# Kernel optimization log

Hardware: AMD Instinct MI355X
Metric: run time of the kernel (lower is better)

The kernel has to match this reference:

```python
import jax, jax.numpy as jnp
import numpy as np

N_EMBD = 1024
N_HEAD = 16
HEAD = N_EMBD // N_HEAD  # 64
N_HIDDEN = 2816          # ((int(2*4*1024/3)-1)//256)*256 + 256
BLOCK_SIZE = 4096
EPS = 1e-5


def rope_cos_sin(T, hd, base=10000.0):
    theta = 1.0 / (base ** (jnp.arange(0, hd, 2, dtype=jnp.float32) / hd))  # (hd/2,)
    idx = jnp.arange(T, dtype=jnp.float32)
    ang = jnp.outer(idx, theta)  # (T, hd/2)
    return jnp.cos(ang), jnp.sin(ang)


def apply_rope(x, cos, sin):
    # x: (B, H, T, hd); rotate interleaved pairs (x0,x1),(x2,x3),...
    xp = x.reshape(*x.shape[:-1], HEAD // 2, 2)
    xe, xo = xp[..., 0], xp[..., 1]
    c = cos[None, None, :, :]
    s = sin[None, None, :, :]
    oe = xe * c - xo * s
    oo = xe * s + xo * c
    return jnp.stack([oe, oo], axis=-1).reshape(x.shape)


def rmsnorm(x, scale):
    ms = jnp.mean(x * x, axis=-1, keepdims=True)
    return scale * (x * jax.lax.rsqrt(ms + EPS))


def setup_inputs() -> dict:
    key = jax.random.key(0)
    ks = jax.random.split(key, 9)
    B, T = 2, 2048
    x = jax.random.normal(ks[0], (B, T, N_EMBD), dtype=jnp.float32)
    y_mask = jax.random.randint(ks[1], (B, 64), 0, 2, dtype=jnp.int32)
    sd = 1.0 / np.sqrt(N_EMBD)
    Wqkv = jax.random.normal(ks[2], (N_EMBD, 3 * N_EMBD), dtype=jnp.float32) * sd
    Wattn_proj = jax.random.normal(ks[3], (N_EMBD, N_EMBD), dtype=jnp.float32) * sd
    scale1 = jnp.ones((N_EMBD,), dtype=jnp.float32)
    scale2 = jnp.ones((N_EMBD,), dtype=jnp.float32)
    Wfc1 = jax.random.normal(ks[4], (N_EMBD, N_HIDDEN), dtype=jnp.float32) * sd
    Wfc2 = jax.random.normal(ks[5], (N_EMBD, N_HIDDEN), dtype=jnp.float32) * sd
    Wmlp_proj = jax.random.normal(ks[6], (N_HIDDEN, N_EMBD), dtype=jnp.float32) / np.sqrt(N_HIDDEN)
    return {"x": x, "y_mask": y_mask, "Wqkv": Wqkv, "Wattn_proj": Wattn_proj,
            "scale1": scale1, "scale2": scale2, "Wfc1": Wfc1, "Wfc2": Wfc2,
            "Wmlp_proj": Wmlp_proj}


def reference(x, y_mask, Wqkv, Wattn_proj, scale1, scale2, Wfc1, Wfc2, Wmlp_proj):
    B, T, C = x.shape
    # ---- attention branch (pre-RMSNorm) ----
    h = rmsnorm(x, scale1)
    qkv = h @ Wqkv  # (B, T, 3C)
    q, k, v = jnp.split(qkv, 3, axis=-1)
    q = q.reshape(B, T, N_HEAD, HEAD).transpose(0, 2, 1, 3)
    k = k.reshape(B, T, N_HEAD, HEAD).transpose(0, 2, 1, 3)
    v = v.reshape(B, T, N_HEAD, HEAD).transpose(0, 2, 1, 3)
    cos, sin = rope_cos_sin(T, HEAD)
    q = apply_rope(q, cos, sin)
    k = apply_rope(k, cos, sin)
    # mixed causal + text-text bidirectional mask
    causal = jnp.tril(jnp.ones((T, T), dtype=bool))  # (T, T)
    ym = y_mask.astype(bool)  # (B, L)
    L = ym.shape[1]
    text = ym[:, :, None] & ym[:, None, :]  # (B, L, L)
    text = jnp.pad(text, ((0, 0), (0, T - L), (0, T - L)))
    mask = jnp.logical_or(causal[None, :, :], text)  # (B, T, T)
    scale = 1.0 / np.sqrt(HEAD)
    scores = jnp.einsum('bhqd,bhkd->bhqk', q, k) * scale
    scores = jnp.where(mask[:, None, :, :], scores, -jnp.inf)
    attn = jax.nn.softmax(scores, axis=-1)
    y = jnp.einsum('bhqk,bhkd->bhqd', attn, v)
    y = y.transpose(0, 2, 1, 3).reshape(B, T, C)
    x = x + y @ Wattn_proj
    # ---- SwiGLU MLP branch (pre-RMSNorm) ----
    h2 = rmsnorm(x, scale2)
    m = jax.nn.silu(h2 @ Wfc1) * (h2 @ Wfc2)
    x = x + m @ Wmlp_proj
    return x
```

## Files before the change

kernel.cpp:

```cpp
#include <hip/hip_runtime.h>
#include <stdint.h>

typedef unsigned short u16;
typedef __attribute__((ext_vector_type(8))) short bf16x8;
typedef __attribute__((ext_vector_type(4))) float f32x4;

__device__ __forceinline__ float b2f(u16 u) {
    union { float f; uint32_t u; } v; v.u = ((uint32_t)u) << 16; return v.f;
}
__device__ __forceinline__ u16 f2b(float f) {
    union { float f; uint32_t u; } v; v.f = f;
    uint32_t r = v.u + 0x7FFFu + ((v.u >> 16) & 1u);
    return (u16)(r >> 16);
}

template <int CTRL>
__device__ __forceinline__ float dppf(float x) {
    union { float f; int i; } u; u.f = x;
    u.i = __builtin_amdgcn_update_dpp(0, u.i, CTRL, 0xF, 0xF, false);
    return u.f;
}
__device__ __forceinline__ float rowmax16(float v) {
    v = fmaxf(v, dppf<0x121>(v));
    v = fmaxf(v, dppf<0x122>(v));
    v = fmaxf(v, dppf<0x124>(v));
    v = fmaxf(v, dppf<0x128>(v));
    return v;
}
__device__ __forceinline__ float rowsum16(float v) {
    v += dppf<0x121>(v);
    v += dppf<0x122>(v);
    v += dppf<0x124>(v);
    v += dppf<0x128>(v);
    return v;
}

__device__ __forceinline__ void stage16(const void* g, void* l) {
    __builtin_amdgcn_global_load_lds(
        (const __attribute__((address_space(1))) uint32_t*)(uintptr_t)g,
        (__attribute__((address_space(3))) uint32_t*)(uint32_t)(uintptr_t)l,
        16, 0, 0);
}

__global__ __launch_bounds__(256) void transpose_all(const float* __restrict__ Wqkv,
                                                     const float* __restrict__ Wattn,
                                                     const float* __restrict__ Wfc1,
                                                     const float* __restrict__ Wfc2,
                                                     const float* __restrict__ Wmlp,
                                                     u16* WtQ, u16* WtA, u16* WtF1,
                                                     u16* WtF2, u16* WtM) {
    __shared__ u16 tile[32][33];
    int id = blockIdx.x;
    const float* src; u16* dst; int R, C;
    if (id < 3072)      {             src = Wqkv;  dst = WtQ;  R = 1024; C = 3072; }
    else if (id < 4096) { id -= 3072; src = Wattn; dst = WtA;  R = 1024; C = 1024; }
    else if (id < 6912) { id -= 4096; src = Wfc1;  dst = WtF1; R = 1024; C = 2816; }
    else if (id < 9728) { id -= 6912; src = Wfc2;  dst = WtF2; R = 1024; C = 2816; }
    else                { id -= 9728; src = Wmlp;  dst = WtM;  R = 2816; C = 1024; }
    const int nbx = C >> 5;
    const int bx = id % nbx, by = id / nbx;
    const int cx = bx * 32, ry = by * 32;
    const int tx = threadIdx.x, ty = threadIdx.y;
    #pragma unroll
    for (int i = 0; i < 32; i += 8)
        tile[ty + i][tx] = f2b(src[(size_t)(ry + ty + i) * C + cx + tx]);
    __syncthreads();
    #pragma unroll
    for (int i = 0; i < 32; i += 8)
        dst[(size_t)(cx + ty + i) * R + ry + tx] = tile[tx][ty + i];
}

__global__ __launch_bounds__(256) void rmsnorm_f32(const float* __restrict__ xin,
                                                   const float* __restrict__ scale,
                                                   u16* __restrict__ out) {
    const int row = blockIdx.x, tid = threadIdx.x;
    const float4 v = ((const float4*)(xin + (size_t)row * 1024))[tid];
    float ss = v.x * v.x + v.y * v.y + v.z * v.z + v.w * v.w;
    #pragma unroll
    for (int d = 32; d; d >>= 1) ss += __shfl_xor(ss, d);
    __shared__ float wsum[4];
    if ((tid & 63) == 0) wsum[tid >> 6] = ss;
    __syncthreads();
    const float r = rsqrtf((wsum[0] + wsum[1] + wsum[2] + wsum[3]) * (1.f / 1024.f) + 1e-5f);
    const float4 sc = ((const float4*)scale)[tid];
    uint2 o;
    o.x = (uint32_t)f2b(v.x * sc.x * r) | ((uint32_t)f2b(v.y * sc.y * r) << 16);
    o.y = (uint32_t)f2b(v.z * sc.z * r) | ((uint32_t)f2b(v.w * sc.w * r) << 16);
    ((uint2*)(out + (size_t)row * 1024))[tid] = o;
}

__global__ __launch_bounds__(256) void rope_kernel(u16* __restrict__ qkv) {
    const int gid = blockIdx.x * 256 + threadIdx.x;
    const int i = gid & 31;
    const int h = (gid >> 5) & 15;
    const int row = gid >> 9;
    const int t = row & 2047;
    const float theta = expf(-(float)i * (9.210340371976184f / 32.0f));
    const float ang = (float)t * theta;
    const float c = cosf(ang), s = sinf(ang);
    const size_t base = (size_t)row * 3072 + h * 64 + 2 * i;
    {
        float xe = b2f(qkv[base]), xo = b2f(qkv[base + 1]);
        qkv[base]     = f2b(xe * c - xo * s);
        qkv[base + 1] = f2b(xe * s + xo * c);
    }
    {
        float xe = b2f(qkv[base + 1024]), xo = b2f(qkv[base + 1025]);
        qkv[base + 1024] = f2b(xe * c - xo * s);
        qkv[base + 1025] = f2b(xe * s + xo * c);
    }
}

template <int EPI>
__global__ __launch_bounds__(256) void gemm_bt(const u16* __restrict__ A,
                                               const u16* __restrict__ Bt,
                                               void* __restrict__ Cout,
                                               const void* __restrict__ Res,
                                               int N, int K) {
    __shared__ __attribute__((aligned(16))) u16 As[2][128 * 32];
    __shared__ __attribute__((aligned(16))) u16 Bs[2][128 * 32];
    const int tid = threadIdx.x;
    const int w = tid >> 6, lane = tid & 63;
    const int quad = lane >> 4, t = lane & 15;
    const int m0 = blockIdx.y * 128, n0 = blockIdx.x * 128;
    const int wm = (w >> 1) * 64, wn = (w & 1) * 64;

    const int srow = w * 16 + (lane >> 2);
    const int scol = (lane & 3) * 8;
    const u16* pA0 = A + (size_t)(m0 + srow) * K + scol;
    const u16* pA1 = pA0 + (size_t)64 * K;
    const u16* pB0 = Bt + (size_t)(n0 + srow) * K + scol;
    const u16* pB1 = pB0 + (size_t)64 * K;

    f32x4 acc[4][4];
    #pragma unroll
    for (int i = 0; i < 4; ++i)
        #pragma unroll
        for (int j = 0; j < 4; ++j) acc[i][j] = (f32x4){0.f, 0.f, 0.f, 0.f};

    for (int kb = 0; kb < K; kb += 64) {
        __syncthreads();
        stage16(pA0 + kb,      (char*)As[0] + w * 1024);
        stage16(pA1 + kb,      (char*)As[0] + 4096 + w * 1024);
        stage16(pB0 + kb,      (char*)Bs[0] + w * 1024);
        stage16(pB1 + kb,      (char*)Bs[0] + 4096 + w * 1024);
        stage16(pA0 + kb + 32, (char*)As[1] + w * 1024);
        stage16(pA1 + kb + 32, (char*)As[1] + 4096 + w * 1024);
        stage16(pB0 + kb + 32, (char*)Bs[1] + w * 1024);
        stage16(pB1 + kb + 32, (char*)Bs[1] + 4096 + w * 1024);
        __syncthreads();
        #pragma unroll
        for (int hf = 0; hf < 2; ++hf) {
            bf16x8 af[4], bfr[4];
            #pragma unroll
            for (int mi = 0; mi < 4; ++mi)
                af[mi] = *(const bf16x8*)((char*)As[hf] + (wm + mi * 16 + t) * 64 + quad * 16);
            #pragma unroll
            for (int ni = 0; ni < 4; ++ni)
                bfr[ni] = *(const bf16x8*)((char*)Bs[hf] + (wn + ni * 16 + t) * 64 + quad * 16);
            #pragma unroll
            for (int mi = 0; mi < 4; ++mi)
                #pragma unroll
                for (int ni = 0; ni < 4; ++ni)
                    acc[mi][ni] = __builtin_amdgcn_mfma_f32_16x16x32_bf16(af[mi], bfr[ni],
                                                                         acc[mi][ni], 0, 0, 0);
        }
    }
    #pragma unroll
    for (int mi = 0; mi < 4; ++mi) {
        const int row0 = m0 + wm + mi * 16 + quad * 4;
        #pragma unroll
        for (int ni = 0; ni < 4; ++ni) {
            const int col = n0 + wn + ni * 16 + t;
            #pragma unroll
            for (int r = 0; r < 4; ++r) {
                const size_t idx = (size_t)(row0 + r) * N + col;
                const float v = acc[mi][ni][r];
                if (EPI == 0) {
                    ((u16*)Cout)[idx] = f2b(v);
                } else if (EPI == 1) {
                    ((float*)Cout)[idx] = v + ((const float*)Res)[idx];
                } else {
                    const float av = b2f(((const u16*)Res)[idx]);
                    ((u16*)Cout)[idx] = f2b((av / (1.f + __expf(-av))) * v);
                }
            }
        }
    }
}

template <int EPI>
__global__ __launch_bounds__(256) void gemm_bt64(const u16* __restrict__ A,
                                                 const u16* __restrict__ Bt,
                                                 void* __restrict__ Cout,
                                                 const float* __restrict__ Res,
                                                 int N, int K) {
    __shared__ __attribute__((aligned(16))) u16 As[2][128 * 32];
    __shared__ __attribute__((aligned(16))) u16 Bs[2][64 * 32];
    const int tid = threadIdx.x;
    const int w = tid >> 6, lane = tid & 63;
    const int quad = lane >> 4, t = lane & 15;
    const int m0 = blockIdx.y * 128, n0 = blockIdx.x * 64;
    const int wm = (w >> 1) * 64, wn = (w & 1) * 32;

    const int srow = w * 16 + (lane >> 2);
    const int scol = (lane & 3) * 8;
    const u16* pA0 = A + (size_t)(m0 + srow) * K + scol;
    const u16* pA1 = pA0 + (size_t)64 * K;
    const u16* pB0 = Bt + (size_t)(n0 + srow) * K + scol;

    f32x4 acc[4][2];
    #pragma unroll
    for (int i = 0; i < 4; ++i)
        #pragma unroll
        for (int j = 0; j < 2; ++j) acc[i][j] = (f32x4){0.f, 0.f, 0.f, 0.f};

    for (int kb = 0; kb < K; kb += 64) {
        __syncthreads();
        stage16(pA0 + kb,      (char*)As[0] + w * 1024);
        stage16(pA1 + kb,      (char*)As[0] + 4096 + w * 1024);
        stage16(pB0 + kb,      (char*)Bs[0] + w * 1024);
        stage16(pA0 + kb + 32, (char*)As[1] + w * 1024);
        stage16(pA1 + kb + 32, (char*)As[1] + 4096 + w * 1024);
        stage16(pB0 + kb + 32, (char*)Bs[1] + w * 1024);
        __syncthreads();
        #pragma unroll
        for (int hf = 0; hf < 2; ++hf) {
            bf16x8 af[4], bfr[2];
            #pragma unroll
            for (int mi = 0; mi < 4; ++mi)
                af[mi] = *(const bf16x8*)((char*)As[hf] + (wm + mi * 16 + t) * 64 + quad * 16);
            #pragma unroll
            for (int ni = 0; ni < 2; ++ni)
                bfr[ni] = *(const bf16x8*)((char*)Bs[hf] + (wn + ni * 16 + t) * 64 + quad * 16);
            #pragma unroll
            for (int mi = 0; mi < 4; ++mi)
                #pragma unroll
                for (int ni = 0; ni < 2; ++ni)
                    acc[mi][ni] = __builtin_amdgcn_mfma_f32_16x16x32_bf16(af[mi], bfr[ni],
                                                                         acc[mi][ni], 0, 0, 0);
        }
    }
    #pragma unroll
    for (int mi = 0; mi < 4; ++mi) {
        const int row0 = m0 + wm + mi * 16 + quad * 4;
        #pragma unroll
        for (int ni = 0; ni < 2; ++ni) {
            const int col = n0 + wn + ni * 16 + t;
            #pragma unroll
            for (int r = 0; r < 4; ++r) {
                const size_t idx = (size_t)(row0 + r) * N + col;
                const float v = acc[mi][ni][r];
                if (EPI == 0) ((u16*)Cout)[idx]   = f2b(v);
                else          ((float*)Cout)[idx] = v + Res[idx];
            }
        }
    }
}

__global__ __launch_bounds__(256) void attn_kernel(const u16* __restrict__ qkv,
                                                   const int* __restrict__ ymask,
                                                   u16* __restrict__ y) {
    const int qt = 31 - blockIdx.x;
    const int h = blockIdx.y, b = blockIdx.z;
    const int tid = threadIdx.x;
    const int w = tid >> 6, lane = tid & 63;
    const int quad = lane >> 4, t = lane & 15;
    const int q0 = qt * 64;

    __shared__ __attribute__((aligned(16))) u16 Ks[64 * 72];
    __shared__ __attribute__((aligned(16))) u16 Vts[64 * 72];
    __shared__ __attribute__((aligned(16))) u16 Ps[4][16 * 72];
    __shared__ int ymL[64];
    if (qt == 0 && tid < 64) ymL[tid] = ymask[b * 64 + tid];

    bf16x8 aQ[2];
    {
        const u16* qp = qkv + (size_t)(b * 2048 + q0 + w * 16 + t) * 3072 + h * 64 + quad * 8;
        aQ[0] = *(const bf16x8*)qp;
        aQ[1] = *(const bf16x8*)(qp + 32);
        #pragma unroll
        for (int i = 0; i < 8; ++i) {
            aQ[0][i] = (short)f2b(b2f((u16)aQ[0][i]) * 0.125f);
            aQ[1][i] = (short)f2b(b2f((u16)aQ[1][i]) * 0.125f);
        }
    }

    const int skey = tid >> 3, sdg = tid & 7;
    const u16* pK = qkv + (size_t)(b * 2048 + skey) * 3072 + h * 64 + sdg * 8 + 1024;
    const int sblk0 = (skey >> 3) ^ sdg;
    const int sblk1 = (4 + (skey >> 3)) ^ sdg;

    f32x4 accO[4] = {(f32x4){0,0,0,0},(f32x4){0,0,0,0},(f32x4){0,0,0,0},(f32x4){0,0,0,0}};
    float mOld[4] = {-INFINITY, -INFINITY, -INFINITY, -INFINITY};
    float lSum[4] = {0.f, 0.f, 0.f, 0.f};

    for (int kb = 0; kb <= qt; ++kb) {
        const u16* pk = pK + (size_t)kb * 196608;
        const uint4 kv0 = *(const uint4*)pk;
        const uint4 vv0 = *(const uint4*)(pk + 1024);
        const uint4 kv1 = *(const uint4*)(pk + 98304);
        const uint4 vv1 = *(const uint4*)(pk + 99328);
        __syncthreads();
        *(uint4*)((char*)Ks + skey * 144 + sdg * 16) = kv0;
        *(uint4*)((char*)Ks + (skey + 32) * 144 + sdg * 16) = kv1;
        {
            const u16* vp0 = (const u16*)&vv0;
            const u16* vp1 = (const u16*)&vv1;
            #pragma unroll
            for (int jj = 0; jj < 8; ++jj) {
                const int row = sdg * 8 + jj;
                Vts[row * 72 + sblk0 * 8 + (skey & 7)] = vp0[jj];
                Vts[row * 72 + sblk1 * 8 + (skey & 7)] = vp1[jj];
            }
        }
        __syncthreads();

        float s[4][4];
        __builtin_amdgcn_s_setprio(1);
        #pragma unroll
        for (int ni = 0; ni < 4; ++ni) {
            bf16x8 bK0 = *(const bf16x8*)((char*)Ks + (ni * 16 + t) * 144 + quad * 16);
            bf16x8 bK1 = *(const bf16x8*)((char*)Ks + (ni * 16 + t) * 144 + 64 + quad * 16);
            f32x4 sa = (f32x4){0.f, 0.f, 0.f, 0.f};
            sa = __builtin_amdgcn_mfma_f32_16x16x32_bf16(aQ[0], bK0, sa, 0, 0, 0);
            sa = __builtin_amdgcn_mfma_f32_16x16x32_bf16(aQ[1], bK1, sa, 0, 0, 0);
            #pragma unroll
            for (int r = 0; r < 4; ++r) s[ni][r] = sa[r];
        }
        __builtin_amdgcn_s_setprio(0);

        if (kb == qt) {
            const int irow = q0 + w * 16 + quad * 4;
            #pragma unroll
            for (int ni = 0; ni < 4; ++ni)
                #pragma unroll
                for (int r = 0; r < 4; ++r) {
                    const int i = irow + r, j = kb * 64 + ni * 16 + t;
                    const bool ok = (j <= i) || (qt == 0 && ymL[i & 63] && ymL[j & 63]);
                    if (!ok) s[ni][r] = -INFINITY;
                }
        }

        float alpha[4];
        bool upd = false;
        #pragma unroll
        for (int r = 0; r < 4; ++r) {
            float mt = fmaxf(fmaxf(s[0][r], s[1][r]), fmaxf(s[2][r], s[3][r]));
            mt = rowmax16(mt);
            const float mNew = fmaxf(mOld[r], mt);
            upd = upd || (mNew > mOld[r]);
            alpha[r] = __expf(mOld[r] - mNew);
            #pragma unroll
            for (int ni = 0; ni < 4; ++ni) s[ni][r] = __expf(s[ni][r] - mNew);
            mOld[r] = mNew;
        }

        u16* Pw = Ps[w];
        #pragma unroll
        for (int ni = 0; ni < 4; ++ni)
            #pragma unroll
            for (int r = 0; r < 4; ++r)
                Pw[(quad * 4 + r) * 72 + ni * 16 + t] = f2b(s[ni][r]);

        #pragma unroll
        for (int r = 0; r < 4; ++r) {
            float rs = (s[0][r] + s[1][r]) + (s[2][r] + s[3][r]);
            rs = rowsum16(rs);
            lSum[r] = lSum[r] * alpha[r] + rs;
        }
        if (__any(upd)) {
            #pragma unroll
            for (int dt = 0; dt < 4; ++dt)
                #pragma unroll
                for (int r = 0; r < 4; ++r) accO[dt][r] *= alpha[r];
        }

        bf16x8 aP0 = *(const bf16x8*)((char*)Pw + t * 144 + quad * 16);
        bf16x8 aP1 = *(const bf16x8*)((char*)Pw + t * 144 + 64 + quad * 16);
        __builtin_amdgcn_s_setprio(1);
        #pragma unroll
        for (int dt = 0; dt < 4; ++dt) {
            const int row = dt * 16 + t, rb = row >> 3;
            bf16x8 bV0 = *(const bf16x8*)((char*)Vts + row * 144 + ((quad ^ rb) << 4));
            bf16x8 bV1 = *(const bf16x8*)((char*)Vts + row * 144 + (((4 + quad) ^ rb) << 4));
            accO[dt] = __builtin_amdgcn_mfma_f32_16x16x32_bf16(aP0, bV0, accO[dt], 0, 0, 0);
            accO[dt] = __builtin_amdgcn_mfma_f32_16x16x32_bf16(aP1, bV1, accO[dt], 0, 0, 0);
        }
        __builtin_amdgcn_s_setprio(0);
    }
    const int orow = q0 + w * 16 + quad * 4;
    #pragma unroll
    for (int dt = 0; dt < 4; ++dt)
        #pragma unroll
        for (int r = 0; r < 4; ++r) {
            const size_t idx = (size_t)(b * 2048 + orow + r) * 1024 + h * 64 + dt * 16 + t;
            y[idx] = f2b(accO[dt][r] / lSum[r]);
        }
}

extern "C" void kernel_launch(void* const* d_in, const int* in_sizes, int n_in,
                              void* d_out, int out_size, void* d_ws, size_t ws_size,
                              hipStream_t stream) {
    const float* x     = (const float*)d_in[0];
    const int*   ym    = (const int*)d_in[1];
    const float* Wqkv  = (const float*)d_in[2];
    const float* Wattn = (const float*)d_in[3];
    const float* s1    = (const float*)d_in[4];
    const float* s2    = (const float*)d_in[5];
    const float* Wfc1  = (const float*)d_in[6];
    const float* Wfc2  = (const float*)d_in[7];
    const float* Wmlp  = (const float*)d_in[8];

    char* ws = (char*)d_ws;
    u16*   h    = (u16*)(ws + 0);
    u16*   qkv  = (u16*)(ws + 8388608);
    u16*   fc1  = qkv;
    float* xr   = (float*)(ws + 33554432);
    u16*   WtA  = (u16*)(ws + 50331648);
    u16*   WtF1 = (u16*)(ws + 52428800);
    u16*   WtF2 = (u16*)(ws + 58195968);
    u16*   WtM  = (u16*)(ws + 63963136);
    u16*   WtQ  = (u16*)(ws + 73400320);
    const dim3 tb(32, 8);

    transpose_all<<<12544, tb, 0, stream>>>(Wqkv, Wattn, Wfc1, Wfc2, Wmlp,
                                            WtQ, WtA, WtF1, WtF2, WtM);
    rmsnorm_f32<<<4096, 256, 0, stream>>>(x, s1, h);
    gemm_bt<0><<<dim3(24, 32), 256, 0, stream>>>(h, WtQ, qkv, nullptr, 3072, 1024);
    rope_kernel<<<8192, 256, 0, stream>>>(qkv);
    attn_kernel<<<dim3(32, 16, 2), 256, 0, stream>>>(qkv, ym, h);
    gemm_bt64<1><<<dim3(16, 32), 256, 0, stream>>>(h, WtA, xr, x, 1024, 1024);
    rmsnorm_f32<<<4096, 256, 0, stream>>>(xr, s2, h);
    gemm_bt<0><<<dim3(22, 32), 256, 0, stream>>>(h, WtF1, fc1, nullptr, 2816, 1024);
    gemm_bt<2><<<dim3(22, 32), 256, 0, stream>>>(h, WtF2, fc1, fc1, 2816, 1024);
    gemm_bt64<1><<<dim3(16, 32), 256, 0, stream>>>(fc1, WtM, (float*)d_out, xr, 1024, 2816);
}
```

Before: 408.8 us.

## Double-buffer V tiles, load K fragments directly from global, and batch RoPE across heads

```diff
diff --git a/kernel.cpp b/kernel.cpp
--- a/kernel.cpp
+++ b/kernel.cpp
@@ -92,22 +92,26 @@
 __global__ __launch_bounds__(256) void rope_kernel(u16* __restrict__ qkv) {
     const int gid = blockIdx.x * 256 + threadIdx.x;
     const int i = gid & 31;
-    const int h = (gid >> 5) & 15;
-    const int row = gid >> 9;
-    const int t = row & 2047;
+    const int row = gid >> 5;
+    const int tpos = row & 2047;
     const float theta = expf(-(float)i * (9.210340371976184f / 32.0f));
-    const float ang = (float)t * theta;
+    const float ang = (float)tpos * theta;
     const float c = cosf(ang), s = sinf(ang);
-    const size_t base = (size_t)row * 3072 + h * 64 + 2 * i;
-    {
-        float xe = b2f(qkv[base]), xo = b2f(qkv[base + 1]);
-        qkv[base]     = f2b(xe * c - xo * s);
-        qkv[base + 1] = f2b(xe * s + xo * c);
-    }
-    {
-        float xe = b2f(qkv[base + 1024]), xo = b2f(qkv[base + 1025]);
-        qkv[base + 1024] = f2b(xe * c - xo * s);
-        qkv[base + 1025] = f2b(xe * s + xo * c);
+    uint32_t* p = (uint32_t*)qkv + (size_t)row * 1536 + i;
+    #pragma unroll
+    for (int h = 0; h < 16; ++h) {
+        const uint32_t uq = p[h * 32];
+        {
+            const float xe = b2f((u16)(uq & 0xffff)), xo = b2f((u16)(uq >> 16));
+            p[h * 32] = (uint32_t)f2b(xe * c - xo * s) |
+                        ((uint32_t)f2b(xe * s + xo * c) << 16);
+        }
+        const uint32_t uk = p[512 + h * 32];
+        {
+            const float xe = b2f((u16)(uk & 0xffff)), xo = b2f((u16)(uk >> 16));
+            p[512 + h * 32] = (uint32_t)f2b(xe * c - xo * s) |
+                              ((uint32_t)f2b(xe * s + xo * c) << 16);
+        }
     }
 }
 
@@ -268,8 +272,7 @@
     const int quad = lane >> 4, t = lane & 15;
     const int q0 = qt * 64;
 
-    __shared__ __attribute__((aligned(16))) u16 Ks[64 * 72];
-    __shared__ __attribute__((aligned(16))) u16 Vts[64 * 72];
+    __shared__ __attribute__((aligned(16))) u16 Vts[2][64 * 72];
     __shared__ __attribute__((aligned(16))) u16 Ps[4][16 * 72];
     __shared__ int ymL[64];
     if (qt == 0 && tid < 64) ymL[tid] = ymask[b * 64 + tid];
@@ -287,44 +290,54 @@
     }
 
     const int skey = tid >> 3, sdg = tid & 7;
-    const u16* pK = qkv + (size_t)(b * 2048 + skey) * 3072 + h * 64 + sdg * 8 + 1024;
+    const u16* pV = qkv + (size_t)(b * 2048 + skey) * 3072 + h * 64 + sdg * 8 + 2048;
     const int sblk0 = (skey >> 3) ^ sdg;
     const int sblk1 = (4 + (skey >> 3)) ^ sdg;
+
+    const u16* pKf = qkv + (size_t)(b * 2048 + t) * 3072 + h * 64 + 1024 + quad * 8;
+
+    {
+        const uint4 vv0 = *(const uint4*)pV;
+        const uint4 vv1 = *(const uint4*)(pV + 98304);
+        const u16* vp0 = (const u16*)&vv0;
+        const u16* vp1 = (const u16*)&vv1;
+        #pragma unroll
+        for (int jj = 0; jj < 8; ++jj) {
+            const int row = sdg * 8 + jj;
+            Vts[0][row * 72 + sblk0 * 8 + (skey & 7)] = vp0[jj];
+            Vts[0][row * 72 + sblk1 * 8 + (skey & 7)] = vp1[jj];
+        }
+    }
+    __syncthreads();
 
     f32x4 accO[4] = {(f32x4){0,0,0,0},(f32x4){0,0,0,0},(f32x4){0,0,0,0},(f32x4){0,0,0,0}};
     float mOld[4] = {-INFINITY, -INFINITY, -INFINITY, -INFINITY};
     float lSum[4] = {0.f, 0.f, 0.f, 0.f};
 
+    int cur = 0;
     for (int kb = 0; kb <= qt; ++kb) {
-        const u16* pk = pK + (size_t)kb * 196608;
-        const uint4 kv0 = *(const uint4*)pk;
-        const uint4 vv0 = *(const uint4*)(pk + 1024);
-        const uint4 kv1 = *(const uint4*)(pk + 98304);
-        const uint4 vv1 = *(const uint4*)(pk + 99328);
-        __syncthreads();
-        *(uint4*)((char*)Ks + skey * 144 + sdg * 16) = kv0;
-        *(uint4*)((char*)Ks + (skey + 32) * 144 + sdg * 16) = kv1;
-        {
-            const u16* vp0 = (const u16*)&vv0;
-            const u16* vp1 = (const u16*)&vv1;
-            #pragma unroll
-            for (int jj = 0; jj < 8; ++jj) {
-                const int row = sdg * 8 + jj;
-                Vts[row * 72 + sblk0 * 8 + (skey & 7)] = vp0[jj];
-                Vts[row * 72 + sblk1 * 8 + (skey & 7)] = vp1[jj];
-            }
-        }
-        __syncthreads();
+        const bool more = (kb < qt);
+        uint4 nv0, nv1;
+        if (more) {
+            const u16* pv = pV + (size_t)(kb + 1) * 196608;
+            nv0 = *(const uint4*)pv;
+            nv1 = *(const uint4*)(pv + 98304);
+        }
+        const u16* pk = pKf + (size_t)kb * 196608;
+        bf16x8 bK0[4], bK1[4];
+        #pragma unroll
+        for (int ni = 0; ni < 4; ++ni) {
+            bK0[ni] = *(const bf16x8*)(pk + (size_t)ni * 49152);
+            bK1[ni] = *(const bf16x8*)(pk + (size_t)ni * 49152 + 32);
+        }
 
         float s[4][4];
         __builtin_amdgcn_s_setprio(1);
         #pragma unroll
         for (int ni = 0; ni < 4; ++ni) {
-            bf16x8 bK0 = *(const bf16x8*)((char*)Ks + (ni * 16 + t) * 144 + quad * 16);
-            bf16x8 bK1 = *(const bf16x8*)((char*)Ks + (ni * 16 + t) * 144 + 64 + quad * 16);
             f32x4 sa = (f32x4){0.f, 0.f, 0.f, 0.f};
-            sa = __builtin_amdgcn_mfma_f32_16x16x32_bf16(aQ[0], bK0, sa, 0, 0, 0);
-            sa = __builtin_amdgcn_mfma_f32_16x16x32_bf16(aQ[1], bK1, sa, 0, 0, 0);
+            sa = __builtin_amdgcn_mfma_f32_16x16x32_bf16(aQ[0], bK0[ni], sa, 0, 0, 0);
+            sa = __builtin_amdgcn_mfma_f32_16x16x32_bf16(aQ[1], bK1[ni], sa, 0, 0, 0);
             #pragma unroll
             for (int r = 0; r < 4; ++r) s[ni][r] = sa[r];
         }
@@ -378,16 +391,32 @@
 
         bf16x8 aP0 = *(const bf16x8*)((char*)Pw + t * 144 + quad * 16);
         bf16x8 aP1 = *(const bf16x8*)((char*)Pw + t * 144 + 64 + quad * 16);
+        const u16* VtsC = Vts[cur];
         __builtin_amdgcn_s_setprio(1);
         #pragma unroll
         for (int dt = 0; dt < 4; ++dt) {
             const int row = dt * 16 + t, rb = row >> 3;
-            bf16x8 bV0 = *(const bf16x8*)((char*)Vts + row * 144 + ((quad ^ rb) << 4));
-            bf16x8 bV1 = *(const bf16x8*)((char*)Vts + row * 144 + (((4 + quad) ^ rb) << 4));
+            bf16x8 bV0 = *(const bf16x8*)((const char*)VtsC + row * 144 + ((quad ^ rb) << 4));
+            bf16x8 bV1 = *(const bf16x8*)((const char*)VtsC + row * 144 + (((4 + quad) ^ rb) << 4));
             accO[dt] = __builtin_amdgcn_mfma_f32_16x16x32_bf16(aP0, bV0, accO[dt], 0, 0, 0);
             accO[dt] = __builtin_amdgcn_mfma_f32_16x16x32_bf16(aP1, bV1, accO[dt], 0, 0, 0);
         }
         __builtin_amdgcn_s_setprio(0);
+
+        if (!more) break;
+        {
+            u16* VtsN = Vts[cur ^ 1];
+            const u16* vp0 = (const u16*)&nv0;
+            const u16* vp1 = (const u16*)&nv1;
+            #pragma unroll
+            for (int jj = 0; jj < 8; ++jj) {
+                const int row = sdg * 8 + jj;
+                VtsN[row * 72 + sblk0 * 8 + (skey & 7)] = vp0[jj];
+                VtsN[row * 72 + sblk1 * 8 + (skey & 7)] = vp1[jj];
+            }
+        }
+        __syncthreads();
+        cur ^= 1;
     }
     const int orow = q0 + w * 16 + quad * 4;
     #pragma unroll
@@ -428,7 +457,7 @@
                                             WtQ, WtA, WtF1, WtF2, WtM);
     rmsnorm_f32<<<4096, 256, 0, stream>>>(x, s1, h);
     gemm_bt<0><<<dim3(24, 32), 256, 0, stream>>>(h, WtQ, qkv, nullptr, 3072, 1024);
-    rope_kernel<<<8192, 256, 0, stream>>>(qkv);
+    rope_kernel<<<512, 256, 0, stream>>>(qkv);
     attn_kernel<<<dim3(32, 16, 2), 256, 0, stream>>>(qkv, ym, h);
     gemm_bt64<1><<<dim3(16, 32), 256, 0, stream>>>(h, WtA, xr, x, 1024, 1024);
     rmsnorm_f32<<<4096, 256, 0, stream>>>(xr, s2, h);
```

Result: slower. 453.5 us (+10.9%).

## Pair causal query tiles per attention block and vectorize RoPE across heads

Applied to the files above, without the earlier changes.

```diff
diff --git a/kernel.cpp b/kernel.cpp
--- a/kernel.cpp
+++ b/kernel.cpp
@@ -92,22 +92,26 @@
 __global__ __launch_bounds__(256) void rope_kernel(u16* __restrict__ qkv) {
     const int gid = blockIdx.x * 256 + threadIdx.x;
     const int i = gid & 31;
-    const int h = (gid >> 5) & 15;
-    const int row = gid >> 9;
-    const int t = row & 2047;
+    const int row = gid >> 5;
+    const int tpos = row & 2047;
     const float theta = expf(-(float)i * (9.210340371976184f / 32.0f));
-    const float ang = (float)t * theta;
+    const float ang = (float)tpos * theta;
     const float c = cosf(ang), s = sinf(ang);
-    const size_t base = (size_t)row * 3072 + h * 64 + 2 * i;
-    {
-        float xe = b2f(qkv[base]), xo = b2f(qkv[base + 1]);
-        qkv[base]     = f2b(xe * c - xo * s);
-        qkv[base + 1] = f2b(xe * s + xo * c);
-    }
-    {
-        float xe = b2f(qkv[base + 1024]), xo = b2f(qkv[base + 1025]);
-        qkv[base + 1024] = f2b(xe * c - xo * s);
-        qkv[base + 1025] = f2b(xe * s + xo * c);
+    uint32_t* p = (uint32_t*)qkv + (size_t)row * 1536 + i;
+    #pragma unroll
+    for (int h = 0; h < 16; ++h) {
+        const uint32_t uq = p[h * 32];
+        {
+            const float xe = b2f((u16)(uq & 0xffff)), xo = b2f((u16)(uq >> 16));
+            p[h * 32] = (uint32_t)f2b(xe * c - xo * s) |
+                        ((uint32_t)f2b(xe * s + xo * c) << 16);
+        }
+        const uint32_t uk = p[512 + h * 32];
+        {
+            const float xe = b2f((u16)(uk & 0xffff)), xo = b2f((u16)(uk >> 16));
+            p[512 + h * 32] = (uint32_t)f2b(xe * c - xo * s) |
+                              ((uint32_t)f2b(xe * s + xo * c) << 16);
+        }
     }
 }
 
@@ -261,142 +265,146 @@
 __global__ __launch_bounds__(256) void attn_kernel(const u16* __restrict__ qkv,
                                                    const int* __restrict__ ymask,
                                                    u16* __restrict__ y) {
-    const int qt = 31 - blockIdx.x;
+    const int pairk = blockIdx.x;
     const int h = blockIdx.y, b = blockIdx.z;
     const int tid = threadIdx.x;
     const int w = tid >> 6, lane = tid & 63;
     const int quad = lane >> 4, t = lane & 15;
-    const int q0 = qt * 64;
 
     __shared__ __attribute__((aligned(16))) u16 Ks[64 * 72];
     __shared__ __attribute__((aligned(16))) u16 Vts[64 * 72];
     __shared__ __attribute__((aligned(16))) u16 Ps[4][16 * 72];
     __shared__ int ymL[64];
-    if (qt == 0 && tid < 64) ymL[tid] = ymask[b * 64 + tid];
-
-    bf16x8 aQ[2];
-    {
-        const u16* qp = qkv + (size_t)(b * 2048 + q0 + w * 16 + t) * 3072 + h * 64 + quad * 8;
-        aQ[0] = *(const bf16x8*)qp;
-        aQ[1] = *(const bf16x8*)(qp + 32);
-        #pragma unroll
-        for (int i = 0; i < 8; ++i) {
-            aQ[0][i] = (short)f2b(b2f((u16)aQ[0][i]) * 0.125f);
-            aQ[1][i] = (short)f2b(b2f((u16)aQ[1][i]) * 0.125f);
-        }
-    }
+    if (pairk == 0 && tid < 64) ymL[tid] = ymask[b * 64 + tid];
 
     const int skey = tid >> 3, sdg = tid & 7;
     const u16* pK = qkv + (size_t)(b * 2048 + skey) * 3072 + h * 64 + sdg * 8 + 1024;
     const int sblk0 = (skey >> 3) ^ sdg;
     const int sblk1 = (4 + (skey >> 3)) ^ sdg;
 
-    f32x4 accO[4] = {(f32x4){0,0,0,0},(f32x4){0,0,0,0},(f32x4){0,0,0,0},(f32x4){0,0,0,0}};
-    float mOld[4] = {-INFINITY, -INFINITY, -INFINITY, -INFINITY};
-    float lSum[4] = {0.f, 0.f, 0.f, 0.f};
-
-    for (int kb = 0; kb <= qt; ++kb) {
-        const u16* pk = pK + (size_t)kb * 196608;
-        const uint4 kv0 = *(const uint4*)pk;
-        const uint4 vv0 = *(const uint4*)(pk + 1024);
-        const uint4 kv1 = *(const uint4*)(pk + 98304);
-        const uint4 vv1 = *(const uint4*)(pk + 99328);
-        __syncthreads();
-        *(uint4*)((char*)Ks + skey * 144 + sdg * 16) = kv0;
-        *(uint4*)((char*)Ks + (skey + 32) * 144 + sdg * 16) = kv1;
+    for (int seg = 0; seg < 2; ++seg) {
+        const int qt = seg ? pairk : 31 - pairk;
+        const int q0 = qt * 64;
+
+        bf16x8 aQ[2];
         {
-            const u16* vp0 = (const u16*)&vv0;
-            const u16* vp1 = (const u16*)&vv1;
-            #pragma unroll
-            for (int jj = 0; jj < 8; ++jj) {
-                const int row = sdg * 8 + jj;
-                Vts[row * 72 + sblk0 * 8 + (skey & 7)] = vp0[jj];
-                Vts[row * 72 + sblk1 * 8 + (skey & 7)] = vp1[jj];
-            }
-        }
-        __syncthreads();
-
-        float s[4][4];
-        __builtin_amdgcn_s_setprio(1);
-        #pragma unroll
-        for (int ni = 0; ni < 4; ++ni) {
-            bf16x8 bK0 = *(const bf16x8*)((char*)Ks + (ni * 16 + t) * 144 + quad * 16);
-            bf16x8 bK1 = *(const bf16x8*)((char*)Ks + (ni * 16 + t) * 144 + 64 + quad * 16);
-            f32x4 sa = (f32x4){0.f, 0.f, 0.f, 0.f};
-            sa = __builtin_amdgcn_mfma_f32_16x16x32_bf16(aQ[0], bK0, sa, 0, 0, 0);
-            sa = __builtin_amdgcn_mfma_f32_16x16x32_bf16(aQ[1], bK1, sa, 0, 0, 0);
-            #pragma unroll
-            for (int r = 0; r < 4; ++r) s[ni][r] = sa[r];
-        }
-        __builtin_amdgcn_s_setprio(0);
-
-        if (kb == qt) {
-            const int irow = q0 + w * 16 + quad * 4;
+            const u16* qp = qkv + (size_t)(b * 2048 + q0 + w * 16 + t) * 3072 + h * 64 + quad * 8;
+            aQ[0] = *(const bf16x8*)qp;
+            aQ[1] = *(const bf16x8*)(qp + 32);
+            #pragma unroll
+            for (int i = 0; i < 8; ++i) {
+                aQ[0][i] = (short)f2b(b2f((u16)aQ[0][i]) * 0.125f);
+                aQ[1][i] = (short)f2b(b2f((u16)aQ[1][i]) * 0.125f);
+            }
+        }
+
+        f32x4 accO[4] = {(f32x4){0,0,0,0},(f32x4){0,0,0,0},(f32x4){0,0,0,0},(f32x4){0,0,0,0}};
+        float mOld[4] = {-INFINITY, -INFINITY, -INFINITY, -INFINITY};
+        float lSum[4] = {0.f, 0.f, 0.f, 0.f};
+
+        for (int kb = 0; kb <= qt; ++kb) {
+            const u16* pk = pK + (size_t)kb * 196608;
+            const uint4 kv0 = *(const uint4*)pk;
+            const uint4 vv0 = *(const uint4*)(pk + 1024);
+            const uint4 kv1 = *(const uint4*)(pk + 98304);
+            const uint4 vv1 = *(const uint4*)(pk + 99328);
+            __syncthreads();
+            *(uint4*)((char*)Ks + skey * 144 + sdg * 16) = kv0;
+            *(uint4*)((char*)Ks + (skey + 32) * 144 + sdg * 16) = kv1;
+            {
+                const u16* vp0 = (const u16*)&vv0;
+                const u16* vp1 = (const u16*)&vv1;
+                #pragma unroll
+                for (int jj = 0; jj < 8; ++jj) {
+                    const int row = sdg * 8 + jj;
+                    Vts[row * 72 + sblk0 * 8 + (skey & 7)] = vp0[jj];
+                    Vts[row * 72 + sblk1 * 8 + (skey & 7)] = vp1[jj];
+                }
+            }
+            __syncthreads();
+
+            float s[4][4];
+            __builtin_amdgcn_s_setprio(1);
+            #pragma unroll
+            for (int ni = 0; ni < 4; ++ni) {
+                bf16x8 bK0 = *(const bf16x8*)((char*)Ks + (ni * 16 + t) * 144 + quad * 16);
+                bf16x8 bK1 = *(const bf16x8*)((char*)Ks + (ni * 16 + t) * 144 + 64 + quad * 16);
+                f32x4 sa = (f32x4){0.f, 0.f, 0.f, 0.f};
+                sa = __builtin_amdgcn_mfma_f32_16x16x32_bf16(aQ[0], bK0, sa, 0, 0, 0);
+                sa = __builtin_amdgcn_mfma_f32_16x16x32_bf16(aQ[1], bK1, sa, 0, 0, 0);
+                #pragma unroll
+                for (int r = 0; r < 4; ++r) s[ni][r] = sa[r];
+            }
+            __builtin_amdgcn_s_setprio(0);
+
+            if (kb == qt) {
+                const int irow = q0 + w * 16 + quad * 4;
+                #pragma unroll
+                for (int ni = 0; ni < 4; ++ni)
+                    #pragma unroll
+                    for (int r = 0; r < 4; ++r) {
+                        const int i = irow + r, j = kb * 64 + ni * 16 + t;
+                        const bool ok = (j <= i) || (qt == 0 && ymL[i & 63] && ymL[j & 63]);
+                        if (!ok) s[ni][r] = -INFINITY;
+                    }
+            }
+
+            float alpha[4];
+            bool upd = false;
+            #pragma unroll
+            for (int r = 0; r < 4; ++r) {
+                float mt = fmaxf(fmaxf(s[0][r], s[1][r]), fmaxf(s[2][r], s[3][r]));
+                mt = rowmax16(mt);
+                const float mNew = fmaxf(mOld[r], mt);
+                upd = upd || (mNew > mOld[r]);
+                alpha[r] = __expf(mOld[r] - mNew);
+                #pragma unroll
+                for (int ni = 0; ni < 4; ++ni) s[ni][r] = __expf(s[ni][r] - mNew);
+                mOld[r] = mNew;
+            }
+
+            u16* Pw = Ps[w];
             #pragma unroll
             for (int ni = 0; ni < 4; ++ni)
                 #pragma unroll
-                for (int r = 0; r < 4; ++r) {
-                    const int i = irow + r, j = kb * 64 + ni * 16 + t;
-                    const bool ok = (j <= i) || (qt == 0 && ymL[i & 63] && ymL[j & 63]);
-                    if (!ok) s[ni][r] = -INFINITY;
-                }
-        }
-
-        float alpha[4];
-        bool upd = false;
-        #pragma unroll
-        for (int r = 0; r < 4; ++r) {
-            float mt = fmaxf(fmaxf(s[0][r], s[1][r]), fmaxf(s[2][r], s[3][r]));
-            mt = rowmax16(mt);
-            const float mNew = fmaxf(mOld[r], mt);
-            upd = upd || (mNew > mOld[r]);
-            alpha[r] = __expf(mOld[r] - mNew);
-            #pragma unroll
-            for (int ni = 0; ni < 4; ++ni) s[ni][r] = __expf(s[ni][r] - mNew);
-            mOld[r] = mNew;
-        }
-
-        u16* Pw = Ps[w];
-        #pragma unroll
-        for (int ni = 0; ni < 4; ++ni)
-            #pragma unroll
-            for (int r = 0; r < 4; ++r)
-                Pw[(quad * 4 + r) * 72 + ni * 16 + t] = f2b(s[ni][r]);
-
-        #pragma unroll
-        for (int r = 0; r < 4; ++r) {
-            float rs = (s[0][r] + s[1][r]) + (s[2][r] + s[3][r]);
-            rs = rowsum16(rs);
-            lSum[r] = lSum[r] * alpha[r] + rs;
-        }
-        if (__any(upd)) {
-            #pragma unroll
-            for (int dt = 0; dt < 4; ++dt)
-                #pragma unroll
-                for (int r = 0; r < 4; ++r) accO[dt][r] *= alpha[r];
-        }
-
-        bf16x8 aP0 = *(const bf16x8*)((char*)Pw + t * 144 + quad * 16);
-        bf16x8 aP1 = *(const bf16x8*)((char*)Pw + t * 144 + 64 + quad * 16);
-        __builtin_amdgcn_s_setprio(1);
-        #pragma unroll
-        for (int dt = 0; dt < 4; ++dt) {
-            const int row = dt * 16 + t, rb = row >> 3;
-            bf16x8 bV0 = *(const bf16x8*)((char*)Vts + row * 144 + ((quad ^ rb) << 4));
-            bf16x8 bV1 = *(const bf16x8*)((char*)Vts + row * 144 + (((4 + quad) ^ rb) << 4));
-            accO[dt] = __builtin_amdgcn_mfma_f32_16x16x32_bf16(aP0, bV0, accO[dt], 0, 0, 0);
-            accO[dt] = __builtin_amdgcn_mfma_f32_16x16x32_bf16(aP1, bV1, accO[dt], 0, 0, 0);
-        }
-        __builtin_amdgcn_s_setprio(0);
-    }
-    const int orow = q0 + w * 16 + quad * 4;
-    #pragma unroll
-    for (int dt = 0; dt < 4; ++dt)
-        #pragma unroll
-        for (int r = 0; r < 4; ++r) {
-            const size_t idx = (size_t)(b * 2048 + orow + r) * 1024 + h * 64 + dt * 16 + t;
-            y[idx] = f2b(accO[dt][r] / lSum[r]);
-        }
+                for (int r = 0; r < 4; ++r)
+                    Pw[(quad * 4 + r) * 72 + ni * 16 + t] = f2b(s[ni][r]);
+
+            #pragma unroll
+            for (int r = 0; r < 4; ++r) {
+                float rs = (s[0][r] + s[1][r]) + (s[2][r] + s[3][r]);
+                rs = rowsum16(rs);
+                lSum[r] = lSum[r] * alpha[r] + rs;
+            }
+            if (__any(upd)) {
+                #pragma unroll
+                for (int dt = 0; dt < 4; ++dt)
+                    #pragma unroll
+                    for (int r = 0; r < 4; ++r) accO[dt][r] *= alpha[r];
+            }
+
+            bf16x8 aP0 = *(const bf16x8*)((char*)Pw + t * 144 + quad * 16);
+            bf16x8 aP1 = *(const bf16x8*)((char*)Pw + t * 144 + 64 + quad * 16);
+            __builtin_amdgcn_s_setprio(1);
+            #pragma unroll
+            for (int dt = 0; dt < 4; ++dt) {
+                const int row = dt * 16 + t, rb = row >> 3;
+                bf16x8 bV0 = *(const bf16x8*)((char*)Vts + row * 144 + ((quad ^ rb) << 4));
+                bf16x8 bV1 = *(const bf16x8*)((char*)Vts + row * 144 + (((4 + quad) ^ rb) << 4));
+                accO[dt] = __builtin_amdgcn_mfma_f32_16x16x32_bf16(aP0, bV0, accO[dt], 0, 0, 0);
+                accO[dt] = __builtin_amdgcn_mfma_f32_16x16x32_bf16(aP1, bV1, accO[dt], 0, 0, 0);
+            }
+            __builtin_amdgcn_s_setprio(0);
+        }
+        const int orow = q0 + w * 16 + quad * 4;
+        #pragma unroll
+        for (int dt = 0; dt < 4; ++dt)
+            #pragma unroll
+            for (int r = 0; r < 4; ++r) {
+                const size_t idx = (size_t)(b * 2048 + orow + r) * 1024 + h * 64 + dt * 16 + t;
+                y[idx] = f2b(accO[dt][r] / lSum[r]);
+            }
+    }
 }
 
 extern "C" void kernel_launch(void* const* d_in, const int* in_sizes, int n_in,
@@ -428,8 +436,8 @@
                                             WtQ, WtA, WtF1, WtF2, WtM);
     rmsnorm_f32<<<4096, 256, 0, stream>>>(x, s1, h);
     gemm_bt<0><<<dim3(24, 32), 256, 0, stream>>>(h, WtQ, qkv, nullptr, 3072, 1024);
-    rope_kernel<<<8192, 256, 0, stream>>>(qkv);
-    attn_kernel<<<dim3(32, 16, 2), 256, 0, stream>>>(qkv, ym, h);
+    rope_kernel<<<512, 256, 0, stream>>>(qkv);
+    attn_kernel<<<dim3(16, 16, 2), 256, 0, stream>>>(qkv, ym, h);
     gemm_bt64<1><<<dim3(16, 32), 256, 0, stream>>>(h, WtA, xr, x, 1024, 1024);
     rmsnorm_f32<<<4096, 256, 0, stream>>>(xr, s2, h);
     gemm_bt<0><<<dim3(22, 32), 256, 0, stream>>>(h, WtF1, fc1, nullptr, 2816, 1024);
```

Result: faster. 372.2 us (-9.0%).
